# Performance work log

Hardware: AMD Instinct MI355X
Metric: run time of the kernel (lower is better)

Reference implementation:

```python
import jax, jax.numpy as jnp
import numpy as np

N_NODES = 100000
N_EDGES = 1600000
IN_DIM = 256
HEADS = 4
OUT_DIM = 32
NEG_SLOPE = 0.2


def setup_inputs() -> dict:
    key = jax.random.key(0)
    ks = jax.random.split(key, 6)
    x = jax.random.normal(ks[0], (N_NODES, IN_DIM), dtype=jnp.float32)
    # xavier-ish init scale for fc and attention vectors
    W = jax.random.normal(ks[1], (IN_DIM, HEADS * OUT_DIM), dtype=jnp.float32) * (1.0 / np.sqrt(IN_DIM))
    attn_l = jax.random.normal(ks[2], (HEADS, OUT_DIM), dtype=jnp.float32) * (1.0 / np.sqrt(OUT_DIM))
    attn_r = jax.random.normal(ks[3], (HEADS, OUT_DIM), dtype=jnp.float32) * (1.0 / np.sqrt(OUT_DIM))
    src = jax.random.randint(ks[4], (N_EDGES,), 0, N_NODES, dtype=jnp.int32)
    dst = jax.random.randint(ks[5], (N_EDGES,), 0, N_NODES, dtype=jnp.int32)
    return {"x": x, "W": W, "attn_l": attn_l, "attn_r": attn_r, "src": src, "dst": dst}


def reference(x, W, attn_l, attn_r, src, dst):
    N = x.shape[0]
    H, D = attn_l.shape
    # shared linear projection (feat_drop = 0)
    feat = (x @ W).reshape(N, H, D)                      # [N,H,D]
    el = jnp.sum(feat * attn_l, axis=-1)                 # [N,H]
    er = jnp.sum(feat * attn_r, axis=-1)                 # [N,H]
    e = jax.nn.leaky_relu(el[src] + er[dst], NEG_SLOPE)  # [E,H]
    # edge softmax over incoming edges of each destination node
    m = jax.ops.segment_max(e, dst, num_segments=N)      # [N,H]
    m = jnp.where(jnp.isfinite(m), m, 0.0)               # zero-in-degree guard
    ex = jnp.exp(e - m[dst])                             # [E,H]
    denom = jax.ops.segment_sum(ex, dst, num_segments=N) # [N,H]
    a = ex / jnp.maximum(denom[dst], 1e-9)               # [E,H] (attn_drop = 0)
    # weighted scatter-add aggregation
    out = jax.ops.segment_sum(a[:, :, None] * feat[src], dst, num_segments=N)  # [N,H,D]
    # head mean (the .mean(1) in GAT1.forward)
    return out.mean(axis=1)                              # [N,D]
```

## Files before the change

### kernel.cpp

```cpp
#include <hip/hip_runtime.h>
#include <math.h>

#define NN 100000
#define NE 1600000
#define IN_DIM 256
#define HD 128
#define NEG_SLOPE 0.2f

#define B1SH 9
#define NPB (1 << B1SH)
#define NB1 ((NN + NPB - 1) / NPB)
#define SC_BLOCKS ((NE / 4 + 1023) / 1024)
#define GEMM_BLOCKS ((NN + 63) / 64)

typedef __attribute__((ext_vector_type(8))) __bf16 bf16x8;
typedef __attribute__((ext_vector_type(4))) float floatx4;
typedef __attribute__((ext_vector_type(2))) float f32x2;

__device__ inline unsigned short f2bf(float f) {
    unsigned int b = __float_as_uint(f);
    b += 0x7fffu + ((b >> 16) & 1u);
    return (unsigned short)(b >> 16);
}
__device__ inline unsigned int pk(float lo, float hi) {
    return (unsigned int)f2bf(lo) | ((unsigned int)f2bf(hi) << 16);
}
__device__ inline float lrelu(float v) { return (v > 0.f) ? v : v * NEG_SLOPE; }
__device__ inline f32x2 un2(unsigned int v) {
    f32x2 r;
    r.x = __uint_as_float(v << 16);
    r.y = __uint_as_float(v & 0xffff0000u);
    return r;
}

__global__ __launch_bounds__(256) void d1_kernel(const float* __restrict__ W,
                                                 unsigned int* __restrict__ wswz,
                                                 const int4* __restrict__ dst4,
                                                 int* __restrict__ gcnt2d) {
    __shared__ int cnt[NB1];
    const int t = threadIdx.x;
    if (blockIdx.x < SC_BLOCKS) {
        for (int i = t; i < NB1; i += 256) cnt[i] = 0;
        __syncthreads();
        int base4 = blockIdx.x * 1024;
#pragma unroll
        for (int k = 0; k < 4; ++k) {
            int gi = base4 + k * 256 + t;
            if (gi < NE / 4) {
                int4 d = dst4[gi];
                atomicAdd(&cnt[d.x >> B1SH], 1);
                atomicAdd(&cnt[d.y >> B1SH], 1);
                atomicAdd(&cnt[d.z >> B1SH], 1);
                atomicAdd(&cnt[d.w >> B1SH], 1);
            }
        }
        __syncthreads();
        for (int i = t; i < NB1; i += 256)
            gcnt2d[blockIdx.x * NB1 + i] = cnt[i];
    } else {
        int g = (blockIdx.x - SC_BLOCKS) * 256 + t;
        int lane = g & 63;
        int tt = (g >> 6) & 7;
        int c = g >> 9;
        int sub = lane & 15, quad = lane >> 4;
        int n = tt * 16 + sub;
        int kbase = c * 32 + quad * 8;
        unsigned int ob = (unsigned int)g * 4;
#pragma unroll
        for (int i = 0; i < 4; ++i) {
            float lo = W[(size_t)(kbase + 2 * i) * HD + n];
            float hi = W[(size_t)(kbase + 2 * i + 1) * HD + n];
            wswz[ob + i] = pk(lo, hi);
        }
    }
}

__global__ __launch_bounds__(256) void d2_kernel(const float* __restrict__ x,
                                                 const uint4* __restrict__ wswz,
                                                 const float* __restrict__ attn_l,
                                                 const float* __restrict__ attn_r,
                                                 unsigned short* __restrict__ featb,
                                                 float* __restrict__ el,
                                                 float* __restrict__ er,
                                                 const int4* __restrict__ src4,
                                                 const int4* __restrict__ dst4,
                                                 const int* __restrict__ gcnt2d,
                                                 unsigned int* __restrict__ pkd,
                                                 int* __restrict__ regstart) {
    __shared__ int cnt[NB1];
    __shared__ int gbase[NB1];
    __shared__ int sh[256];
    const int t = threadIdx.x;

    if (blockIdx.x < SC_BLOCKS) {
        const int b = blockIdx.x;
        int colsum = 0, mypre = 0;
        if (t < NB1) {
            for (int bb = 0; bb < SC_BLOCKS; ++bb) {
                int v = gcnt2d[bb * NB1 + t];
                colsum += v;
                if (bb < b) mypre += v;
            }
        }
        sh[t] = (t < NB1) ? colsum : 0;
        __syncthreads();
        for (int o = 1; o < 256; o <<= 1) {
            int a = (t >= o) ? sh[t - o] : 0;
            __syncthreads();
            sh[t] += a;
            __syncthreads();
        }
        int rstart = sh[t] - ((t < NB1) ? colsum : 0);
        if (t < NB1) gbase[t] = rstart + mypre;
        if (b == 0 && t < NB1) regstart[t] = rstart;
        if (b == 0 && t == 0) regstart[NB1] = NE;
        for (int i = t; i < NB1; i += 256) cnt[i] = 0;
        __syncthreads();

        int base4 = b * 1024;
        unsigned int pkv[16];
        unsigned int brk[16];
#pragma unroll
        for (int k = 0; k < 4; ++k) {
            int gi = base4 + k * 256 + t;
            bool ok = gi < NE / 4;
            int gic = ok ? gi : 0;
            int4 s = src4[gic];
            int4 d = dst4[gic];
            int dd[4] = {d.x, d.y, d.z, d.w};
            int ss[4] = {s.x, s.y, s.z, s.w};
#pragma unroll
            for (int j4 = 0; j4 < 4; ++j4) {
                int e = k * 4 + j4;
                if (ok) {
                    int bk = dd[j4] >> B1SH;
                    int r = atomicAdd(&cnt[bk], 1);
                    brk[e] = ((unsigned int)bk << 12) | (unsigned int)r;
                    pkv[e] = ((unsigned int)(dd[j4] & (NPB - 1)) << 17) | (unsigned int)ss[j4];
                } else {
                    brk[e] = 0xFFFFFFFFu;
                }
            }
        }
        __syncthreads();
#pragma unroll
        for (int e = 0; e < 16; ++e) {
            if (brk[e] != 0xFFFFFFFFu) {
                int bk = brk[e] >> 12;
                int r = brk[e] & 0xFFF;
                pkd[gbase[bk] + r] = pkv[e];
            }
        }
    } else {
        const int lane = t & 63, wv = t >> 6;
        const int sub = lane & 15, quad = lane >> 4;
        const int row0 = (blockIdx.x - SC_BLOCKS) * 64 + wv * 16;

        int m = row0 + sub;
        if (m >= NN) m = NN - 1;
        const float* xp = x + (size_t)m * IN_DIM + quad * 8;

        bf16x8 af[8];
#pragma unroll
        for (int h = 0; h < 2; ++h) {
            float4 raw[4][2];
#pragma unroll
            for (int c = 0; c < 4; ++c) {
                raw[c][0] = *(const float4*)(xp + (h * 4 + c) * 32);
                raw[c][1] = *(const float4*)(xp + (h * 4 + c) * 32 + 4);
            }
#pragma unroll
            for (int c = 0; c < 4; ++c) {
                uint4 au;
                au.x = pk(raw[c][0].x, raw[c][0].y);
                au.y = pk(raw[c][0].z, raw[c][0].w);
                au.z = pk(raw[c][1].x, raw[c][1].y);
                au.w = pk(raw[c][1].z, raw[c][1].w);
                af[h * 4 + c] = __builtin_bit_cast(bf16x8, au);
            }
        }

        floatx4 acc[8];
#pragma unroll
        for (int tt = 0; tt < 8; ++tt) acc[tt] = (floatx4){0.f, 0.f, 0.f, 0.f};

#pragma unroll
        for (int c = 0; c < 8; ++c) {
            uint4 bu[8];
#pragma unroll
            for (int tt = 0; tt < 8; ++tt) bu[tt] = wswz[(c * 8 + tt) * 64 + lane];
#pragma unroll
            for (int tt = 0; tt < 8; ++tt) {
                bf16x8 bfr = __builtin_bit_cast(bf16x8, bu[tt]);
                acc[tt] = __builtin_amdgcn_mfma_f32_16x16x32_bf16(af[c], bfr, acc[tt], 0, 0, 0);
            }
        }

        float al[8], ar[8];
#pragma unroll
        for (int tt = 0; tt < 8; ++tt) {
            al[tt] = attn_l[tt * 16 + sub];
            ar[tt] = attn_r[tt * 16 + sub];
        }

#pragma unroll
        for (int r = 0; r < 4; ++r) {
            int row = row0 + quad * 4 + r;
            uint4 fv;
            fv.x = pk(acc[0][r], acc[1][r]);
            fv.y = pk(acc[2][r], acc[3][r]);
            fv.z = pk(acc[4][r], acc[5][r]);
            fv.w = pk(acc[6][r], acc[7][r]);
            float pl[4], pr[4];
#pragma unroll
            for (int hh = 0; hh < 4; ++hh) {
                pl[hh] = acc[2 * hh][r] * al[2 * hh] + acc[2 * hh + 1][r] * al[2 * hh + 1];
                pr[hh] = acc[2 * hh][r] * ar[2 * hh] + acc[2 * hh + 1][r] * ar[2 * hh + 1];
            }
#pragma unroll
            for (int o = 1; o < 16; o <<= 1) {
#pragma unroll
                for (int hh = 0; hh < 4; ++hh) {
                    pl[hh] += __shfl_xor(pl[hh], o);
                    pr[hh] += __shfl_xor(pr[hh], o);
                }
            }
            if (row < NN) {
                *(uint4*)(featb + (size_t)row * HD + sub * 8) = fv;
                if (sub < 4) {
                    float vl = (sub == 0) ? pl[0] : (sub == 1) ? pl[1] : (sub == 2) ? pl[2] : pl[3];
                    float vr = (sub == 0) ? pr[0] : (sub == 1) ? pr[1] : (sub == 2) ? pr[2] : pr[3];
                    el[row * 4 + sub] = vl;
                    er[row * 4 + sub] = vr;
                }
            }
        }
    }
}

__global__ __launch_bounds__(256) void build_kernel(const unsigned int* __restrict__ pkd,
                                                    const int* __restrict__ regstart,
                                                    int* __restrict__ offs,
                                                    int* __restrict__ csr_src) {
    __shared__ int fcnt[NPB];
    __shared__ int foffs[NPB];
    __shared__ int ssc[256];
    int b = blockIdx.x, t = threadIdx.x;
    int rs = regstart[b], re = regstart[b + 1];
    int n = re - rs;
    if (b == 0 && t == 0) offs[NN] = NE;

    for (int i = t; i < NPB; i += 256) fcnt[i] = 0;
    __syncthreads();
    for (int i = t; i < n; i += 256) {
        unsigned int v = pkd[rs + i];
        atomicAdd(&fcnt[v >> 17], 1);
    }
    __syncthreads();
    int a0 = fcnt[2 * t], a1 = fcnt[2 * t + 1];
    int s = a0 + a1;
    ssc[t] = s;
    __syncthreads();
    for (int o = 1; o < 256; o <<= 1) {
        int u = (t >= o) ? ssc[t - o] : 0;
        __syncthreads();
        ssc[t] += u;
        __syncthreads();
    }
    int excl = ssc[t] - s;
    foffs[2 * t] = excl;
    foffs[2 * t + 1] = excl + a0;
    __syncthreads();
#pragma unroll
    for (int q = 0; q < 2; ++q) {
        int j = t + q * 256;
        int node = b * NPB + j;
        if (node < NN) offs[node] = rs + foffs[j];
    }
    for (int i = t; i < NPB; i += 256) fcnt[i] = 0;
    __syncthreads();
    int i = t;
    for (; i + 768 < n; i += 1024) {
        unsigned int v0 = pkd[rs + i];
        unsigned int v1 = pkd[rs + i + 256];
        unsigned int v2 = pkd[rs + i + 512];
        unsigned int v3 = pkd[rs + i + 768];
        int j0 = v0 >> 17, j1 = v1 >> 17, j2 = v2 >> 17, j3 = v3 >> 17;
        int r0 = atomicAdd(&fcnt[j0], 1);
        int r1 = atomicAdd(&fcnt[j1], 1);
        int r2 = atomicAdd(&fcnt[j2], 1);
        int r3 = atomicAdd(&fcnt[j3], 1);
        csr_src[rs + foffs[j0] + r0] = (int)(v0 & 0x1FFFFu);
        csr_src[rs + foffs[j1] + r1] = (int)(v1 & 0x1FFFFu);
        csr_src[rs + foffs[j2] + r2] = (int)(v2 & 0x1FFFFu);
        csr_src[rs + foffs[j3] + r3] = (int)(v3 & 0x1FFFFu);
    }
    for (; i < n; i += 256) {
        unsigned int v = pkd[rs + i];
        int j = v >> 17;
        int r = atomicAdd(&fcnt[j], 1);
        csr_src[rs + foffs[j] + r] = (int)(v & 0x1FFFFu);
    }
}

#define CH 32
__global__ __launch_bounds__(256, 4) void aggregate_kernel(const uint4* __restrict__ featu4,
                                                           const float4* __restrict__ el4,
                                                           const float4* __restrict__ er4,
                                                           const int* __restrict__ offs,
                                                           const int* __restrict__ csr_src,
                                                           float* __restrict__ out) {
    __shared__ int    s_sv[4][4][CH + 1];
    __shared__ float4 s_a4[4][4][CH + 1];
    __shared__ int sdeg[16], smap[16];

    const int tid = threadIdx.x;
    const int lane = tid & 63, wv = tid >> 6;
    const int g = lane >> 4, sub = lane & 15;

    if (tid < 16) {
        int n0 = blockIdx.x * 16 + tid;
        sdeg[tid] = offs[n0 + 1] - offs[n0];
    }
    __syncthreads();
    if (tid < 16) {
        int d = sdeg[tid];
        int rank = 0;
#pragma unroll
        for (int j = 0; j < 16; ++j) {
            int dj = sdeg[j];
            rank += (dj < d) || (dj == d && j < tid);
        }
        smap[rank] = blockIdx.x * 16 + tid;
    }
    __syncthreads();
    const int node = smap[wv * 4 + g];
    const int beg = offs[node], end = offs[node + 1];

    const float4 erv = er4[node];
    float4 sm = make_float4(0.f, 0.f, 0.f, 0.f);
    f32x2 acc2[4];
#pragma unroll
    for (int i = 0; i < 4; ++i) acc2[i] = (f32x2){0.f, 0.f};

    for (int c0 = beg; c0 < end; c0 += CH) {
        int cnt = end - c0;
        if (cnt > CH) cnt = CH;

        int svr[2];
#pragma unroll
        for (int t = 0; t < 2; ++t) {
            int slot = sub + t * 16;
            int sv = (slot < cnt) ? csr_src[c0 + slot] : 0;
            svr[t] = sv;
            s_sv[wv][g][slot] = sv * 16;
        }

        uint4 ua[8], ub[8];
#pragma unroll
        for (int e = 0; e < 8; ++e)
            ua[e] = featu4[(size_t)s_sv[wv][g][e] + sub];

#pragma unroll
        for (int t = 0; t < 2; ++t) {
            int slot = sub + t * 16;
            float4 w = make_float4(0.f, 0.f, 0.f, 0.f);
            if (slot < cnt) {
                float4 e = el4[svr[t]];
                w.x = __expf(lrelu(e.x + erv.x));
                w.y = __expf(lrelu(e.y + erv.y));
                w.z = __expf(lrelu(e.z + erv.z));
                w.w = __expf(lrelu(e.w + erv.w));
                sm.x += w.x; sm.y += w.y; sm.z += w.z; sm.w += w.w;
            }
            s_a4[wv][g][slot] = w;
        }

        int rounds = (cnt + 7) >> 3;
        int jr = 0;
        while (true) {
            bool m1 = (jr + 1) < rounds;
            if (m1) {
                int nb = (jr + 1) << 3;
#pragma unroll
                for (int e = 0; e < 8; ++e)
                    ub[e] = featu4[(size_t)s_sv[wv][g][nb + e] + sub];
            }
            {
                int jb = jr << 3;
#pragma unroll
                for (int e = 0; e < 8; ++e) {
                    float4 we = s_a4[wv][g][jb + e];
                    uint4 u = ua[e];
                    f32x2 w0 = {we.x, we.x}, w1 = {we.y, we.y};
                    f32x2 w2 = {we.z, we.z}, w3 = {we.w, we.w};
                    acc2[0] = __builtin_elementwise_fma(w0, un2(u.x), acc2[0]);
                    acc2[1] = __builtin_elementwise_fma(w1, un2(u.y), acc2[1]);
                    acc2[2] = __builtin_elementwise_fma(w2, un2(u.z), acc2[2]);
                    acc2[3] = __builtin_elementwise_fma(w3, un2(u.w), acc2[3]);
                }
            }
            ++jr;
            if (!m1) break;
            bool m2 = (jr + 1) < rounds;
            if (m2) {
                int nb = (jr + 1) << 3;
#pragma unroll
                for (int e = 0; e < 8; ++e)
                    ua[e] = featu4[(size_t)s_sv[wv][g][nb + e] + sub];
            }
            {
                int jb = jr << 3;
#pragma unroll
                for (int e = 0; e < 8; ++e) {
                    float4 we = s_a4[wv][g][jb + e];
                    uint4 u = ub[e];
                    f32x2 w0 = {we.x, we.x}, w1 = {we.y, we.y};
                    f32x2 w2 = {we.z, we.z}, w3 = {we.w, we.w};
                    acc2[0] = __builtin_elementwise_fma(w0, un2(u.x), acc2[0]);
                    acc2[1] = __builtin_elementwise_fma(w1, un2(u.y), acc2[1]);
                    acc2[2] = __builtin_elementwise_fma(w2, un2(u.z), acc2[2]);
                    acc2[3] = __builtin_elementwise_fma(w3, un2(u.w), acc2[3]);
                }
            }
            ++jr;
            if (!m2) break;
        }
    }

#pragma unroll
    for (int o = 1; o < 16; o <<= 1) {
        sm.x += __shfl_xor(sm.x, o);
        sm.y += __shfl_xor(sm.y, o);
        sm.z += __shfl_xor(sm.z, o);
        sm.w += __shfl_xor(sm.w, o);
    }
    float ix = 1.f / fmaxf(sm.x, 1e-9f);
    float iy = 1.f / fmaxf(sm.y, 1e-9f);
    float iz = 1.f / fmaxf(sm.z, 1e-9f);
    float iw = 1.f / fmaxf(sm.w, 1e-9f);
    float ox = 0.25f * (acc2[0].x * ix + acc2[1].x * iy + acc2[2].x * iz + acc2[3].x * iw);
    float oy = 0.25f * (acc2[0].y * ix + acc2[1].y * iy + acc2[2].y * iz + acc2[3].y * iw);
    out[node * 32 + sub]      = ox;
    out[node * 32 + 16 + sub] = oy;
}

extern "C" void kernel_launch(void* const* d_in, const int* in_sizes, int n_in,
                              void* d_out, int out_size, void* d_ws, size_t ws_size,
                              hipStream_t stream) {
    const float* x      = (const float*)d_in[0];
    const float* W      = (const float*)d_in[1];
    const float* attn_l = (const float*)d_in[2];
    const float* attn_r = (const float*)d_in[3];
    const int*   src    = (const int*)d_in[4];
    const int*   dst    = (const int*)d_in[5];
    float* out = (float*)d_out;

    char* p = (char*)d_ws;
    auto alloc = [&](size_t bytes) -> void* {
        void* r = (void*)p;
        p += (bytes + 255) & ~(size_t)255;
        return r;
    };
    unsigned short* featb = (unsigned short*)alloc((size_t)NN * HD * 2);
    unsigned int*   wswz  = (unsigned int*)alloc(4096 * 16);
    float* el      = (float*)alloc((size_t)NN * 4 * 4);
    float* er      = (float*)alloc((size_t)NN * 4 * 4);
    int*   offs    = (int*)alloc((size_t)(NN + 1) * 4);
    unsigned int* pkd = (unsigned int*)alloc((size_t)NE * 4);
    int*   csr     = (int*)alloc((size_t)NE * 4);
    int*   gcnt2d  = (int*)alloc((size_t)SC_BLOCKS * NB1 * 4);
    int*   regstart= (int*)alloc((size_t)(NB1 + 1) * 4);

    d1_kernel<<<SC_BLOCKS + 16, 256, 0, stream>>>(W, wswz, (const int4*)dst, gcnt2d);
    d2_kernel<<<SC_BLOCKS + GEMM_BLOCKS, 256, 0, stream>>>(x, (const uint4*)wswz, attn_l, attn_r,
                                                           featb, el, er,
                                                           (const int4*)src, (const int4*)dst,
                                                           gcnt2d, pkd, regstart);
    build_kernel<<<NB1, 256, 0, stream>>>(pkd, regstart, offs, csr);
    aggregate_kernel<<<NN / 16, 256, 0, stream>>>((const uint4*)featb, (const float4*)el,
                                                  (const float4*)er, offs, csr, out);
}
```

Measured before the change: 284.5 us.

## Transpose block-count matrix, interleave scatter and GEMM blocks, widen build kernel

The per-block bucket counts are now stored transposed and padded (SCP=392), so each scatter block reads its column with contiguous int4 loads instead of strided scalar loads. In d2, scatter blocks are interleaved with GEMM blocks (every fifth block), which spreads the heavier scan work across CUs instead of putting it all at the start of the grid. The build kernel moves to 1024 threads with a single-element-per-thread scan over 512 buckets. Risks are idle early-exit blocks in the padded grid and more barriers in the wider scan.

```diff
diff --git a/kernel.cpp b/kernel.cpp
--- a/kernel.cpp
+++ b/kernel.cpp
@@ -11,7 +11,9 @@
 #define NPB (1 << B1SH)
 #define NB1 ((NN + NPB - 1) / NPB)
 #define SC_BLOCKS ((NE / 4 + 1023) / 1024)
+#define SCP 392
 #define GEMM_BLOCKS ((NN + 63) / 64)
+#define D2_GRID (SC_BLOCKS * 5)
 
 typedef __attribute__((ext_vector_type(8))) __bf16 bf16x8;
 typedef __attribute__((ext_vector_type(4))) float floatx4;
@@ -36,7 +38,7 @@
 __global__ __launch_bounds__(256) void d1_kernel(const float* __restrict__ W,
                                                  unsigned int* __restrict__ wswz,
                                                  const int4* __restrict__ dst4,
-                                                 int* __restrict__ gcnt2d) {
+                                                 int* __restrict__ gcnt2dT) {
     __shared__ int cnt[NB1];
     const int t = threadIdx.x;
     if (blockIdx.x < SC_BLOCKS) {
@@ -56,7 +58,10 @@
         }
         __syncthreads();
         for (int i = t; i < NB1; i += 256)
-            gcnt2d[blockIdx.x * NB1 + i] = cnt[i];
+            gcnt2dT[i * SCP + blockIdx.x] = cnt[i];
+        if (blockIdx.x == 0)
+            for (int i = t; i < NB1; i += 256)
+                gcnt2dT[i * SCP + SC_BLOCKS] = 0;
     } else {
         int g = (blockIdx.x - SC_BLOCKS) * 256 + t;
         int lane = g & 63;
@@ -84,22 +89,34 @@
                                                  float* __restrict__ er,
                                                  const int4* __restrict__ src4,
                                                  const int4* __restrict__ dst4,
-                                                 const int* __restrict__ gcnt2d,
+                                                 const int* __restrict__ gcnt2dT,
                                                  unsigned int* __restrict__ pkd,
                                                  int* __restrict__ regstart) {
     __shared__ int cnt[NB1];
     __shared__ int gbase[NB1];
     __shared__ int sh[256];
     const int t = threadIdx.x;
-
-    if (blockIdx.x < SC_BLOCKS) {
-        const int b = blockIdx.x;
+    const int bid = blockIdx.x;
+
+    if (bid % 5 == 0) {
+        const int b = bid / 5;
         int colsum = 0, mypre = 0;
         if (t < NB1) {
-            for (int bb = 0; bb < SC_BLOCKS; ++bb) {
-                int v = gcnt2d[bb * NB1 + t];
-                colsum += v;
-                if (bb < b) mypre += v;
+            const int4* rowp = (const int4*)(gcnt2dT + t * SCP);
+#pragma unroll 7
+            for (int q = 0; q < SCP / 4; ++q) {
+                int4 v = rowp[q];
+                int s4 = v.x + v.y + v.z + v.w;
+                colsum += s4;
+                int base = q * 4;
+                if (base + 4 <= b) {
+                    mypre += s4;
+                } else {
+                    if (base + 0 < b) mypre += v.x;
+                    if (base + 1 < b) mypre += v.y;
+                    if (base + 2 < b) mypre += v.z;
+                    if (base + 3 < b) mypre += v.w;
+                }
             }
         }
         sh[t] = (t < NB1) ? colsum : 0;
@@ -152,9 +169,11 @@
             }
         }
     } else {
+        const int gb = bid - 1 - bid / 5;
+        if (gb >= GEMM_BLOCKS) return;
         const int lane = t & 63, wv = t >> 6;
         const int sub = lane & 15, quad = lane >> 4;
-        const int row0 = (blockIdx.x - SC_BLOCKS) * 64 + wv * 16;
+        const int row0 = gb * 64 + wv * 16;
 
         int m = row0 + sub;
         if (m >= NN) m = NN - 1;
@@ -238,53 +257,48 @@
     }
 }
 
-__global__ __launch_bounds__(256) void build_kernel(const unsigned int* __restrict__ pkd,
-                                                    const int* __restrict__ regstart,
-                                                    int* __restrict__ offs,
-                                                    int* __restrict__ csr_src) {
+__global__ __launch_bounds__(1024) void build_kernel(const unsigned int* __restrict__ pkd,
+                                                     const int* __restrict__ regstart,
+                                                     int* __restrict__ offs,
+                                                     int* __restrict__ csr_src) {
     __shared__ int fcnt[NPB];
     __shared__ int foffs[NPB];
-    __shared__ int ssc[256];
+    __shared__ int ssc[NPB];
     int b = blockIdx.x, t = threadIdx.x;
     int rs = regstart[b], re = regstart[b + 1];
     int n = re - rs;
     if (b == 0 && t == 0) offs[NN] = NE;
 
-    for (int i = t; i < NPB; i += 256) fcnt[i] = 0;
-    __syncthreads();
-    for (int i = t; i < n; i += 256) {
+    if (t < NPB) fcnt[t] = 0;
+    __syncthreads();
+    for (int i = t; i < n; i += 1024) {
         unsigned int v = pkd[rs + i];
         atomicAdd(&fcnt[v >> 17], 1);
     }
     __syncthreads();
-    int a0 = fcnt[2 * t], a1 = fcnt[2 * t + 1];
-    int s = a0 + a1;
-    ssc[t] = s;
-    __syncthreads();
-    for (int o = 1; o < 256; o <<= 1) {
-        int u = (t >= o) ? ssc[t - o] : 0;
-        __syncthreads();
-        ssc[t] += u;
-        __syncthreads();
-    }
-    int excl = ssc[t] - s;
-    foffs[2 * t] = excl;
-    foffs[2 * t + 1] = excl + a0;
-    __syncthreads();
-#pragma unroll
-    for (int q = 0; q < 2; ++q) {
-        int j = t + q * 256;
-        int node = b * NPB + j;
-        if (node < NN) offs[node] = rs + foffs[j];
-    }
-    for (int i = t; i < NPB; i += 256) fcnt[i] = 0;
+    int a = 0;
+    if (t < NPB) { a = fcnt[t]; ssc[t] = a; }
+    __syncthreads();
+    for (int o = 1; o < NPB; o <<= 1) {
+        int u = 0;
+        if (t < NPB && t >= o) u = ssc[t - o];
+        __syncthreads();
+        if (t < NPB) ssc[t] += u;
+        __syncthreads();
+    }
+    if (t < NPB) {
+        foffs[t] = ssc[t] - a;
+        int node = b * NPB + t;
+        if (node < NN) offs[node] = rs + foffs[t];
+        fcnt[t] = 0;
+    }
     __syncthreads();
     int i = t;
-    for (; i + 768 < n; i += 1024) {
+    for (; i + 3072 < n; i += 4096) {
         unsigned int v0 = pkd[rs + i];
-        unsigned int v1 = pkd[rs + i + 256];
-        unsigned int v2 = pkd[rs + i + 512];
-        unsigned int v3 = pkd[rs + i + 768];
+        unsigned int v1 = pkd[rs + i + 1024];
+        unsigned int v2 = pkd[rs + i + 2048];
+        unsigned int v3 = pkd[rs + i + 3072];
         int j0 = v0 >> 17, j1 = v1 >> 17, j2 = v2 >> 17, j3 = v3 >> 17;
         int r0 = atomicAdd(&fcnt[j0], 1);
         int r1 = atomicAdd(&fcnt[j1], 1);
@@ -295,7 +309,7 @@
         csr_src[rs + foffs[j2] + r2] = (int)(v2 & 0x1FFFFu);
         csr_src[rs + foffs[j3] + r3] = (int)(v3 & 0x1FFFFu);
     }
-    for (; i < n; i += 256) {
+    for (; i < n; i += 1024) {
         unsigned int v = pkd[rs + i];
         int j = v >> 17;
         int r = atomicAdd(&fcnt[j], 1);
@@ -469,15 +483,15 @@
     int*   offs    = (int*)alloc((size_t)(NN + 1) * 4);
     unsigned int* pkd = (unsigned int*)alloc((size_t)NE * 4);
     int*   csr     = (int*)alloc((size_t)NE * 4);
-    int*   gcnt2d  = (int*)alloc((size_t)SC_BLOCKS * NB1 * 4);
+    int*   gcnt2dT = (int*)alloc((size_t)NB1 * SCP * 4);
     int*   regstart= (int*)alloc((size_t)(NB1 + 1) * 4);
 
-    d1_kernel<<<SC_BLOCKS + 16, 256, 0, stream>>>(W, wswz, (const int4*)dst, gcnt2d);
-    d2_kernel<<<SC_BLOCKS + GEMM_BLOCKS, 256, 0, stream>>>(x, (const uint4*)wswz, attn_l, attn_r,
-                                                           featb, el, er,
-                                                           (const int4*)src, (const int4*)dst,
-                                                           gcnt2d, pkd, regstart);
-    build_kernel<<<NB1, 256, 0, stream>>>(pkd, regstart, offs, csr);
+    d1_kernel<<<SC_BLOCKS + 16, 256, 0, stream>>>(W, wswz, (const int4*)dst, gcnt2dT);
+    d2_kernel<<<D2_GRID, 256, 0, stream>>>(x, (const uint4*)wswz, attn_l, attn_r,
+                                           featb, el, er,
+                                           (const int4*)src, (const int4*)dst,
+                                           gcnt2dT, pkd, regstart);
+    build_kernel<<<NB1, 1024, 0, stream>>>(pkd, regstart, offs, csr);
     aggregate_kernel<<<NN / 16, 256, 0, stream>>>((const uint4*)featb, (const float4*)el,
                                                   (const float4*)er, offs, csr, out);
 }
```

Measured after the change: 301.5 us. +6.0%, slower.
